# Kernel tuning notes

Hardware: AMD Instinct MI355X
Metric: run time of the kernel (lower is better)

## Reference

```python
import jax, jax.numpy as jnp
import numpy as np

N_NODES = 50000
N_EDGES = 800000
D = 64


def setup_inputs() -> dict:
    key = jax.random.key(0)
    k1, k2, k3, k4, k5 = jax.random.split(key, 5)
    x = jax.random.normal(k1, (N_NODES, D), dtype=jnp.float32)
    edge_index = jax.random.randint(k2, (2, N_EDGES), 0, N_NODES, dtype=jnp.int64)
    edge_weight = jax.random.uniform(k3, (N_EDGES,), dtype=jnp.float32)
    W = jax.random.normal(k4, (D, D), dtype=jnp.float32) / np.sqrt(D)
    b = jax.random.normal(k5, (D,), dtype=jnp.float32) * 0.01
    return {"x": x, "edge_index": edge_index, "edge_weight": edge_weight, "W": W, "b": b}


def reference(x, edge_index, edge_weight, W, b):
    # GCNConv (PyG defaults): add self-loops (weight 1), symmetric normalization,
    # linear transform then normalized scatter-add aggregation, bias, then ReLU.
    n = x.shape[0]
    loop = jnp.arange(n, dtype=edge_index.dtype)
    src = jnp.concatenate([edge_index[0], loop])          # [E+N] message sources
    dst = jnp.concatenate([edge_index[1], loop])          # [E+N] message targets
    ew = jnp.concatenate([edge_weight, jnp.ones((n,), dtype=x.dtype)])
    # degree on target nodes from edge weights
    deg = jax.ops.segment_sum(ew, dst, num_segments=n)
    dinv = jnp.where(deg > 0, jax.lax.rsqrt(deg), 0.0)
    norm = dinv[src] * ew * dinv[dst]                      # [E+N]
    h = x @ W                                              # [N, D] linear first
    msg = h[src] * norm[:, None]                           # gather + scale
    out = jax.ops.segment_sum(msg, dst, num_segments=n) + b
    return jax.nn.relu(out)
```

## Files before the change

### kernel.cpp

```cpp
#include <hip/hip_runtime.h>

#define N_NODES 50000
#define N_EDGES 800000
#define D 64
#define NBUCK 782
#define BINBLK 512
#define EPB 1563
#define ECHUNK 7
#define GEMMBLK ((N_NODES + 15) / 16)
#define CAP 1536
#define FIXSCALE 4194304.0f


__device__ inline unsigned short f2bf(float f) {
    unsigned u = __float_as_uint(f);
    unsigned r = (u + 0x7FFFu + ((u >> 16) & 1u)) >> 16;
    return (unsigned short)r;
}
__device__ inline float bf2f(unsigned short h) {
    return __uint_as_float(((unsigned)h) << 16);
}
__device__ inline int wave_incl_scan(int v, int lane) {
#pragma unroll
    for (int off = 1; off < 64; off <<= 1) {
        int n = __shfl_up(v, off, 64);
        if (lane >= off) v += n;
    }
    return v;
}


__global__ void k_zero(int* __restrict__ gcur) {
    int i = blockIdx.x * blockDim.x + threadIdx.x;
    if (i < NBUCK) gcur[i] = 0;
}

union ShU {
    int lh[NBUCK];
    struct { float Ws[D][D]; float Xs[4][D]; } gm;
};
__global__ __launch_bounds__(256) void k_bin_gemm(
        const int* __restrict__ src, const int* __restrict__ dst,
        const float* __restrict__ ew,
        int* __restrict__ gcur, unsigned long long* __restrict__ binned,
        const float* __restrict__ x, const float* __restrict__ W,
        unsigned short* __restrict__ hb) {
    __shared__ ShU sh;
    int t = threadIdx.x;
    if (blockIdx.x < BINBLK) {
        int rd[ECHUNK]; int rs[ECHUNK]; float rw[ECHUNK];
        int* lh = sh.lh;
        for (int i = t; i < NBUCK; i += 256) lh[i] = 0;
        __syncthreads();
        int base = blockIdx.x * EPB;
#pragma unroll
        for (int i = 0; i < ECHUNK; ++i) {
            int k = i * 256 + t;
            rd[i] = -1;
            if (k < EPB) {
                int e = base + k;
                if (e < N_EDGES) {
                    rd[i] = dst[e];
                    rs[i] = src[e];
                    rw[i] = ew[e];
                    atomicAdd(&lh[rd[i] >> 6], 1);
                }
            }
        }
        __syncthreads();
        for (int i = t; i < NBUCK; i += 256) {
            int c = lh[i];
            lh[i] = (c > 0) ? atomicAdd(&gcur[i], c) : 0;
        }
        __syncthreads();
#pragma unroll
        for (int i = 0; i < ECHUNK; ++i) {
            if (rd[i] >= 0) {
                int bkt = rd[i] >> 6;
                int pos = atomicAdd(&lh[bkt], 1);
                if (pos < CAP)
                    binned[(size_t)bkt * CAP + pos] =
                        ((unsigned long long)__float_as_uint(rw[i]) << 32)
                      | ((unsigned)rs[i] << 16) | (unsigned)rd[i];
            }
        }
    } else {
        float (*Ws)[D] = sh.gm.Ws;
        float (*Xs)[D] = sh.gm.Xs;
        for (int k = t; k < D * D; k += 256) Ws[k / D][k % D] = W[k];
        int base = (blockIdx.x - BINBLK) * 16;
        int r = t >> 6, c = t & 63;
        for (int g = 0; g < 4; ++g) {
            int row = base + g * 4 + r;
            __syncthreads();
            Xs[r][c] = (row < N_NODES) ? x[(size_t)row * D + c] : 0.0f;
            __syncthreads();
            float acc = 0.0f;
#pragma unroll
            for (int k = 0; k < D; ++k) acc = fmaf(Xs[r][k], Ws[k][c], acc);
            if (row < N_NODES) hb[(size_t)row * D + c] = f2bf(acc);
        }
    }
}

__global__ void k_sortbucket(const unsigned long long* __restrict__ binned,
                             const int* __restrict__ gcur,
                             unsigned* __restrict__ csr,
                             unsigned* __restrict__ rc,
                             float* __restrict__ dinv) {
    __shared__ unsigned long long stage[CAP];
    __shared__ unsigned long long cw[64];
    __shared__ int off2[64];
    int t = threadIdx.x;
    if (t < 64) cw[t] = 0ULL;
    __syncthreads();
    int b = blockIdx.x;
    size_t beg = (size_t)b * CAP;
    int len = min(gcur[b], CAP);
    for (int k = t; k < len; k += 256) {
        unsigned long long p = binned[beg + k];
        stage[k] = p;
        int dl = (int)(p & 63);
        float w = __uint_as_float((unsigned)(p >> 32));
        atomicAdd(&cw[dl], (1ULL << 40) | (unsigned long long)__float2uint_rn(w * FIXSCALE));
    }
    __syncthreads();
    if (t < 64) {
        int c = (int)(cw[t] >> 40);
        float wfix = (float)(cw[t] & ((1ULL << 40) - 1ULL));
        int inc = wave_incl_scan(c, t);
        int excl = inc - c;
        off2[t] = excl;
        int node = b * 64 + t;
        if (node < N_NODES) {
            rc[node] = ((unsigned)c << 12) | (unsigned)excl;
            dinv[node] = rsqrtf(1.0f + wfix * (1.0f / FIXSCALE));
        }
    }
    __syncthreads();
    for (int k = t; k < len; k += 256) {
        unsigned long long p = stage[k];
        int dl = (int)(p & 63);
        int r = atomicAdd(&off2[dl], 1);
        unsigned short ewb = f2bf(__uint_as_float((unsigned)(p >> 32)));
        csr[beg + r] = ((unsigned)ewb << 16) | (unsigned)((p >> 16) & 0xffffu);
    }
}

__global__ void k_aggregate(const unsigned short* __restrict__ hb,
                            const float* __restrict__ dinv,
                            const unsigned* __restrict__ rc,
                            const unsigned* __restrict__ csr,
                            const float* __restrict__ bias,
                            float* __restrict__ out) {
    int node = blockIdx.x * 4 + (threadIdx.x >> 6);
    int lane = threadIdx.x & 63;
    if (node >= N_NODES) return;
    int half = lane >> 5;
    int cl = lane & 31;
    float di = dinv[node];
    unsigned r = rc[node];
    int cnt = (int)(r >> 12);
    size_t beg = (size_t)(node >> 6) * CAP + (r & 0xFFFu);
    float a0 = 0.0f, a1 = 0.0f, p0 = 0.0f, p1 = 0.0f;
    {
        unsigned hd = *(const unsigned*)(hb + (size_t)node * D + 2 * cl);
        float m = (half == 0) ? di : 0.0f;
        a0 = m * bf2f((unsigned short)hd);
        a1 = m * bf2f((unsigned short)(hd >> 16));
    }
    for (int b0 = 0; b0 < cnt; b0 += 64) {
        int n = min(64, cnt - b0);
        int my_src = 0;
        float my_ew = 0.0f;
        if (lane < n) {
            unsigned q = csr[beg + b0 + lane];
            my_src = (int)(q & 0xffffu);
            my_ew = bf2f((unsigned short)(q >> 16)) * dinv[my_src];
        }
        int jp = 0;
        for (; jp + 3 < n; jp += 4) {
            int iA = jp + half, iB = jp + 2 + half;
            int sA = __shfl(my_src, iA, 64);
            float eA = __shfl(my_ew, iA, 64);
            int sB = __shfl(my_src, iB, 64);
            float eB = __shfl(my_ew, iB, 64);
            unsigned hA = *(const unsigned*)(hb + (size_t)sA * D + 2 * cl);
            unsigned hB = *(const unsigned*)(hb + (size_t)sB * D + 2 * cl);
            a0 = fmaf(bf2f((unsigned short)hA), eA, a0);
            a1 = fmaf(bf2f((unsigned short)(hA >> 16)), eA, a1);
            p0 = fmaf(bf2f((unsigned short)hB), eB, p0);
            p1 = fmaf(bf2f((unsigned short)(hB >> 16)), eB, p1);
        }
        for (; jp + 1 < n; jp += 2) {
            int iA = jp + half;
            int sA = __shfl(my_src, iA, 64);
            float eA = __shfl(my_ew, iA, 64);
            unsigned hA = *(const unsigned*)(hb + (size_t)sA * D + 2 * cl);
            a0 = fmaf(bf2f((unsigned short)hA), eA, a0);
            a1 = fmaf(bf2f((unsigned short)(hA >> 16)), eA, a1);
        }
        if (jp < n) {
            int sA = __shfl(my_src, jp, 64);
            float eA = __shfl(my_ew, jp, 64);
            unsigned hA = *(const unsigned*)(hb + (size_t)sA * D + 2 * cl);
            float m = (half == 0) ? eA : 0.0f;
            a0 = fmaf(bf2f((unsigned short)hA), m, a0);
            a1 = fmaf(bf2f((unsigned short)(hA >> 16)), m, a1);
        }
    }
    a0 += p0; a1 += p1;
    a0 += __shfl_xor(a0, 32, 64);
    a1 += __shfl_xor(a1, 32, 64);
    if (half == 0) {
        float v0 = fmaf(di, a0, bias[2 * cl]);
        float v1 = fmaf(di, a1, bias[2 * cl + 1]);
        float2 o;
        o.x = fmaxf(v0, 0.0f);
        o.y = fmaxf(v1, 0.0f);
        *(float2*)(out + (size_t)node * D + 2 * cl) = o;
    }
}


extern "C" void kernel_launch(void* const* d_in, const int* in_sizes, int n_in,
                              void* d_out, int out_size, void* d_ws, size_t ws_size,
                              hipStream_t stream) {
    const float* x  = (const float*)d_in[0];
    const int*   ei = (const int*)d_in[1];
    const float* ew = (const float*)d_in[2];
    const float* W  = (const float*)d_in[3];
    const float* b  = (const float*)d_in[4];
    float* out = (float*)d_out;

    const int* src = ei;
    const int* dst = ei + N_EDGES;

    unsigned long long* binned = (unsigned long long*)d_ws;
    unsigned* csr      = (unsigned*)(binned + (size_t)NBUCK * CAP);
    int*   gcur        = (int*)(csr + (size_t)NBUCK * CAP);
    unsigned* rc       = (unsigned*)(gcur + 1024);
    float* dinv        = (float*)(rc + 50048);
    unsigned short* hb = (unsigned short*)(dinv + 50048);

    dim3 blk(256);
    k_zero<<<4, blk, 0, stream>>>(gcur);
    k_bin_gemm<<<BINBLK + GEMMBLK, blk, 0, stream>>>(src, dst, ew, gcur, binned,
                                                     x, W, hb);
    k_sortbucket<<<NBUCK, blk, 0, stream>>>(binned, gcur, csr, rc, dinv);
    k_aggregate<<<(N_NODES + 3) / 4, blk, 0, stream>>>(hb, dinv, rc, csr, b, out);
}
```

Measured before the change: 83.07 us.

## Move GEMM co-scheduling from binning kernel into bucket-sort kernel

The dense x@W GEMM blocks were co-launched with the edge binning kernel. They now run alongside the per-bucket sort kernel, and binning becomes its own small kernel. The aim is to hide the GEMM behind the sort stage rather than the binning stage, which may balance the load between the two launches better. The cost is a larger shared-memory union for the sort blocks (about 12.8KB staging versus 16KB for the GEMM), which may change occupancy.

```diff
diff --git a/kernel.cpp b/kernel.cpp
--- a/kernel.cpp
+++ b/kernel.cpp
@@ -35,60 +35,107 @@
     if (i < NBUCK) gcur[i] = 0;
 }
 
+__global__ __launch_bounds__(256) void k_bin(
+        const int* __restrict__ src, const int* __restrict__ dst,
+        const float* __restrict__ ew,
+        int* __restrict__ gcur, unsigned long long* __restrict__ binned) {
+    __shared__ int lh[NBUCK];
+    int t = threadIdx.x;
+    int rd[ECHUNK]; int rs[ECHUNK]; float rw[ECHUNK];
+    for (int i = t; i < NBUCK; i += 256) lh[i] = 0;
+    __syncthreads();
+    int base = blockIdx.x * EPB;
+#pragma unroll
+    for (int i = 0; i < ECHUNK; ++i) {
+        int k = i * 256 + t;
+        rd[i] = -1;
+        if (k < EPB) {
+            int e = base + k;
+            if (e < N_EDGES) {
+                rd[i] = dst[e];
+                rs[i] = src[e];
+                rw[i] = ew[e];
+                atomicAdd(&lh[rd[i] >> 6], 1);
+            }
+        }
+    }
+    __syncthreads();
+    for (int i = t; i < NBUCK; i += 256) {
+        int c = lh[i];
+        lh[i] = (c > 0) ? atomicAdd(&gcur[i], c) : 0;
+    }
+    __syncthreads();
+#pragma unroll
+    for (int i = 0; i < ECHUNK; ++i) {
+        if (rd[i] >= 0) {
+            int bkt = rd[i] >> 6;
+            int pos = atomicAdd(&lh[bkt], 1);
+            if (pos < CAP)
+                binned[(size_t)bkt * CAP + pos] =
+                    ((unsigned long long)__float_as_uint(rw[i]) << 32)
+                  | ((unsigned)rs[i] << 16) | (unsigned)rd[i];
+        }
+    }
+}
+
 union ShU {
-    int lh[NBUCK];
+    struct { unsigned long long stage[CAP];
+             unsigned long long cw[64]; int off2[64]; } so;
     struct { float Ws[D][D]; float Xs[4][D]; } gm;
 };
-__global__ __launch_bounds__(256) void k_bin_gemm(
-        const int* __restrict__ src, const int* __restrict__ dst,
-        const float* __restrict__ ew,
-        int* __restrict__ gcur, unsigned long long* __restrict__ binned,
+__global__ __launch_bounds__(256) void k_sortgemm(
+        const unsigned long long* __restrict__ binned,
+        const int* __restrict__ gcur,
+        unsigned* __restrict__ csr, unsigned* __restrict__ rc,
+        float* __restrict__ dinv,
         const float* __restrict__ x, const float* __restrict__ W,
         unsigned short* __restrict__ hb) {
     __shared__ ShU sh;
     int t = threadIdx.x;
-    if (blockIdx.x < BINBLK) {
-        int rd[ECHUNK]; int rs[ECHUNK]; float rw[ECHUNK];
-        int* lh = sh.lh;
-        for (int i = t; i < NBUCK; i += 256) lh[i] = 0;
+    int bid = blockIdx.x;
+    if (bid < NBUCK) {
+        unsigned long long* stage = sh.so.stage;
+        unsigned long long* cw = sh.so.cw;
+        int* off2 = sh.so.off2;
+        if (t < 64) cw[t] = 0ULL;
         __syncthreads();
-        int base = blockIdx.x * EPB;
-#pragma unroll
-        for (int i = 0; i < ECHUNK; ++i) {
-            int k = i * 256 + t;
-            rd[i] = -1;
-            if (k < EPB) {
-                int e = base + k;
-                if (e < N_EDGES) {
-                    rd[i] = dst[e];
-                    rs[i] = src[e];
-                    rw[i] = ew[e];
-                    atomicAdd(&lh[rd[i] >> 6], 1);
-                }
+        int b = bid;
+        size_t beg = (size_t)b * CAP;
+        int len = min(gcur[b], CAP);
+        for (int k = t; k < len; k += 256) {
+            unsigned long long p = binned[beg + k];
+            stage[k] = p;
+            int dl = (int)(p & 63);
+            float w = __uint_as_float((unsigned)(p >> 32));
+            atomicAdd(&cw[dl],
+                      (1ULL << 40) | (unsigned long long)__float2uint_rn(w * FIXSCALE));
+        }
+        __syncthreads();
+        if (t < 64) {
+            int c = (int)(cw[t] >> 40);
+            float wfix = (float)(cw[t] & ((1ULL << 40) - 1ULL));
+            int inc = wave_incl_scan(c, t);
+            int excl = inc - c;
+            off2[t] = excl;
+            int node = b * 64 + t;
+            if (node < N_NODES) {
+                rc[node] = ((unsigned)c << 12) | (unsigned)excl;
+                dinv[node] = rsqrtf(1.0f + wfix * (1.0f / FIXSCALE));
             }
         }
         __syncthreads();
-        for (int i = t; i < NBUCK; i += 256) {
-            int c = lh[i];
-            lh[i] = (c > 0) ? atomicAdd(&gcur[i], c) : 0;
-        }
-        __syncthreads();
-#pragma unroll
-        for (int i = 0; i < ECHUNK; ++i) {
-            if (rd[i] >= 0) {
-                int bkt = rd[i] >> 6;
-                int pos = atomicAdd(&lh[bkt], 1);
-                if (pos < CAP)
-                    binned[(size_t)bkt * CAP + pos] =
-                        ((unsigned long long)__float_as_uint(rw[i]) << 32)
-                      | ((unsigned)rs[i] << 16) | (unsigned)rd[i];
-            }
+        for (int k = t; k < len; k += 256) {
+            unsigned long long p = stage[k];
+            int dl = (int)(p & 63);
+            int r = atomicAdd(&off2[dl], 1);
+            unsigned short ewb = f2bf(__uint_as_float((unsigned)(p >> 32)));
+            csr[beg + r] = ((unsigned)ewb << 16) | (unsigned)((p >> 16) & 0xffffu);
         }
     } else {
         float (*Ws)[D] = sh.gm.Ws;
         float (*Xs)[D] = sh.gm.Xs;
         for (int k = t; k < D * D; k += 256) Ws[k / D][k % D] = W[k];
-        int base = (blockIdx.x - BINBLK) * 16;
+        int base = (bid - NBUCK) * 16;
         int r = t >> 6, c = t & 63;
         for (int g = 0; g < 4; ++g) {
             int row = base + g * 4 + r;
@@ -100,50 +147,6 @@
             for (int k = 0; k < D; ++k) acc = fmaf(Xs[r][k], Ws[k][c], acc);
             if (row < N_NODES) hb[(size_t)row * D + c] = f2bf(acc);
         }
-    }
-}
-
-__global__ void k_sortbucket(const unsigned long long* __restrict__ binned,
-                             const int* __restrict__ gcur,
-                             unsigned* __restrict__ csr,
-                             unsigned* __restrict__ rc,
-                             float* __restrict__ dinv) {
-    __shared__ unsigned long long stage[CAP];
-    __shared__ unsigned long long cw[64];
-    __shared__ int off2[64];
-    int t = threadIdx.x;
-    if (t < 64) cw[t] = 0ULL;
-    __syncthreads();
-    int b = blockIdx.x;
-    size_t beg = (size_t)b * CAP;
-    int len = min(gcur[b], CAP);
-    for (int k = t; k < len; k += 256) {
-        unsigned long long p = binned[beg + k];
-        stage[k] = p;
-        int dl = (int)(p & 63);
-        float w = __uint_as_float((unsigned)(p >> 32));
-        atomicAdd(&cw[dl], (1ULL << 40) | (unsigned long long)__float2uint_rn(w * FIXSCALE));
-    }
-    __syncthreads();
-    if (t < 64) {
-        int c = (int)(cw[t] >> 40);
-        float wfix = (float)(cw[t] & ((1ULL << 40) - 1ULL));
-        int inc = wave_incl_scan(c, t);
-        int excl = inc - c;
-        off2[t] = excl;
-        int node = b * 64 + t;
-        if (node < N_NODES) {
-            rc[node] = ((unsigned)c << 12) | (unsigned)excl;
-            dinv[node] = rsqrtf(1.0f + wfix * (1.0f / FIXSCALE));
-        }
-    }
-    __syncthreads();
-    for (int k = t; k < len; k += 256) {
-        unsigned long long p = stage[k];
-        int dl = (int)(p & 63);
-        int r = atomicAdd(&off2[dl], 1);
-        unsigned short ewb = f2bf(__uint_as_float((unsigned)(p >> 32)));
-        csr[beg + r] = ((unsigned)ewb << 16) | (unsigned)((p >> 16) & 0xffffu);
     }
 }
 
@@ -245,8 +248,8 @@
 
     dim3 blk(256);
     k_zero<<<4, blk, 0, stream>>>(gcur);
-    k_bin_gemm<<<BINBLK + GEMMBLK, blk, 0, stream>>>(src, dst, ew, gcur, binned,
-                                                     x, W, hb);
-    k_sortbucket<<<NBUCK, blk, 0, stream>>>(binned, gcur, csr, rc, dinv);
+    k_bin<<<BINBLK, blk, 0, stream>>>(src, dst, ew, gcur, binned);
+    k_sortgemm<<<NBUCK + GEMMBLK, blk, 0, stream>>>(binned, gcur, csr, rc, dinv,
+                                                    x, W, hb);
     k_aggregate<<<(N_NODES + 3) / 4, blk, 0, stream>>>(hb, dinv, rc, csr, b, out);
 }
```

Measured after the change: 89.70 us. +8.0%, slower.
